# Performance work log

Hardware: AMD Instinct MI355X
Metric: run time of the kernel (lower is better)

Reference implementation:

```python
import jax, jax.numpy as jnp
import numpy as np

N_NODES = 100000
N_EDGES = 1600000
D_FEAT = 256
UNITS = 128


def setup_inputs() -> dict:
    key = jax.random.key(0)
    k1, k2, k3, k4, k5 = jax.random.split(key, 5)
    x = jax.random.normal(k1, (N_NODES, D_FEAT), dtype=jnp.float32)
    # glorot-scale init for w (scale doesn't affect correctness checking)
    w = jax.random.normal(k2, (D_FEAT, UNITS), dtype=jnp.float32) * (2.0 / (D_FEAT + UNITS)) ** 0.5
    adj_src = jax.random.randint(k3, (N_EDGES,), 0, N_NODES, dtype=jnp.int64)
    adj_dst = jax.random.randint(k4, (N_EDGES,), 0, N_NODES, dtype=jnp.int64)
    adj_vals = jax.random.uniform(k5, (N_EDGES,), dtype=jnp.float32)
    return {"x": x, "w": w, "adj_src": adj_src, "adj_dst": adj_dst, "adj_vals": adj_vals}


def reference(x, w, adj_src, adj_dst, adj_vals):
    # x: [N, D], w: [D, U]  -> dense projection
    h = x @ w  # [N, U]
    # sparse_dense_matmul(adj_norm, h): out[i] = sum_j A[i,j] * h[j]
    # COO: edge e contributes adj_vals[e] * h[adj_src[e]] to row adj_dst[e]
    msgs = adj_vals[:, None] * h[adj_src]  # [E, U]
    out = jax.ops.segment_sum(msgs, adj_dst, num_segments=N_NODES)  # [N, U]
    return out
```

## Files before the change

### kernel.cpp

```cpp
#include <hip/hip_runtime.h>

#define D_FEAT 256
#define UNITS  128

#define NBITS  7
#define BINSZ  128
#define BINCAP 2432
#define MAXNB  800

typedef __attribute__((ext_vector_type(8))) short short8;
typedef __attribute__((ext_vector_type(4))) float floatx4;

__device__ inline ushort f2bf(float f) {
    uint u = __float_as_uint(f);
    uint r = u + 0x7FFF + ((u >> 16) & 1);
    return (ushort)(r >> 16);
}

__global__ __launch_bounds__(256) void wt_prep_kernel(const float* __restrict__ w,
                                                      ushort* __restrict__ wT) {
    int idx = blockIdx.x * 256 + threadIdx.x;
    int n = idx >> 8;
    int k = idx & 255;
    wT[n * 256 + k] = f2bf(w[(size_t)k * UNITS + n]);
}

__global__ __launch_bounds__(256, 2) void gemm_mfma2_kernel(const float* __restrict__ x,
                                                            const ushort* __restrict__ wT,
                                                            ushort* __restrict__ hb, int M) {
    const int tid  = threadIdx.x;
    const int wave = tid >> 6;
    const int lane = tid & 63;
    const int quad = lane >> 4;
    const int m16  = lane & 15;

    const int row  = blockIdx.x * 64 + wave * 16 + m16;
    const int rowc = row < M ? row : M - 1;
    const float* xr = x + (size_t)rowc * D_FEAT;

    float4 xv[16];
    #pragma unroll
    for (int s = 0; s < 8; ++s) {
        const float4* p = (const float4*)(xr + s * 32 + quad * 8);
        xv[2 * s]     = p[0];
        xv[2 * s + 1] = p[1];
    }

    short8 afrag[8];
    #pragma unroll
    for (int s = 0; s < 8; ++s) {
        float4 lo = xv[2 * s];
        float4 hi = xv[2 * s + 1];
        union { short8 v; ushort u[8]; } af;
        af.u[0] = f2bf(lo.x); af.u[1] = f2bf(lo.y);
        af.u[2] = f2bf(lo.z); af.u[3] = f2bf(lo.w);
        af.u[4] = f2bf(hi.x); af.u[5] = f2bf(hi.y);
        af.u[6] = f2bf(hi.z); af.u[7] = f2bf(hi.w);
        afrag[s] = af.v;
    }

    floatx4 acc[8] = {};
    #pragma unroll
    for (int s = 0; s < 8; ++s) {
        #pragma unroll
        for (int c = 0; c < 8; ++c) {
            short8 bfrag = *(const short8*)&wT[(c * 16 + m16) * 256 + s * 32 + quad * 8];
            acc[c] = __builtin_amdgcn_mfma_f32_16x16x32_bf16(afrag[s], bfrag, acc[c], 0, 0, 0);
        }
    }

    #pragma unroll
    for (int c = 0; c < 8; ++c) {
        #pragma unroll
        for (int i = 0; i < 4; ++i) {
            int r = blockIdx.x * 64 + wave * 16 + quad * 4 + i;
            if (r < M) hb[(size_t)r * UNITS + c * 16 + m16] = f2bf(acc[c][i]);
        }
    }
}

__global__ __launch_bounds__(1024) void coarse_scatter_kernel(const int* __restrict__ src,
                                                              const int* __restrict__ dst,
                                                              const float* __restrict__ vals,
                                                              int* __restrict__ cursor,
                                                              int2* __restrict__ staged,
                                                              int E, int NB, int chunk) {
    __shared__ int s_hist[MAXNB];
    __shared__ int s_base[MAXNB];

    const int tid = threadIdx.x;
    const int T   = 1024;
    const int e0 = blockIdx.x * chunk;
    const int e1 = min(E, e0 + chunk);

    for (int i = tid; i < NB; i += T) s_hist[i] = 0;
    __syncthreads();

    for (int e = e0 + tid; e < e1; e += T)
        atomicAdd(&s_hist[dst[e] >> NBITS], 1);
    __syncthreads();

    for (int b = tid; b < NB; b += T) {
        int c = s_hist[b];
        s_base[b] = (c > 0) ? atomicAdd(&cursor[b * 4], c) : 0;
    }
    __syncthreads();
    for (int i = tid; i < NB; i += T) s_hist[i] = 0;
    __syncthreads();

    for (int e = e0 + tid; e < e1; e += T) {
        int d = dst[e];
        int b = d >> NBITS;
        int r = s_base[b] + atomicAdd(&s_hist[b], 1);
        if (r < BINCAP) {
            int meta = src[e] | ((d & (BINSZ - 1)) << 20);
            staged[(size_t)b * BINCAP + r] = make_int2(meta, __float_as_int(vals[e]));
        }
    }
}

__global__ __launch_bounds__(256) void gather_sort_kernel(const int* __restrict__ cursor,
                                                          const int2* __restrict__ staged,
                                                          const ushort* __restrict__ hb,
                                                          float* __restrict__ out, int N) {
    __shared__ int2 sbuf[BINCAP];
    __shared__ int cnt[BINSZ], ofs[BINSZ], cur[BINSZ];
    __shared__ int gofs[16];

    const int b   = blockIdx.x;
    const int tid = threadIdx.x;

    int n = cursor[b * 4];
    if (n > BINCAP) n = BINCAP;

    for (int i = tid; i < BINSZ; i += 256) cnt[i] = 0;
    __syncthreads();

    const int2* sg = staged + (size_t)b * BINCAP;

    for (int i = tid; i < n; i += 256)
        atomicAdd(&cnt[(sg[i].x >> 20) & (BINSZ - 1)], 1);
    __syncthreads();

    if (tid < 16) {
        int s = 0;
        #pragma unroll
        for (int j = 0; j < 8; ++j) s += cnt[tid * 8 + j];
        gofs[tid] = s;
    }
    __syncthreads();
    if (tid == 0) {
        int run = 0;
        #pragma unroll
        for (int g = 0; g < 16; ++g) { int c = gofs[g]; gofs[g] = run; run += c; }
    }
    __syncthreads();
    if (tid < 16) {
        int run = gofs[tid];
        #pragma unroll
        for (int j = 0; j < 8; ++j) {
            int d = tid * 8 + j;
            int c = cnt[d];
            ofs[d] = run; cur[d] = run; run += c;
        }
    }
    __syncthreads();

    for (int i = tid; i < n; i += 256) {
        int2 e = sg[i];
        int pos = atomicAdd(&cur[(e.x >> 20) & (BINSZ - 1)], 1);
        sbuf[pos] = e;
    }
    __syncthreads();

    const int half = tid >> 5;
    const int lane = tid & 31;

    for (int d0 = 0; d0 < BINSZ; d0 += 8) {
        int d  = d0 + half;
        int dg = b * BINSZ + d;
        if (dg >= N) continue;
        int start = ofs[d];
        int c     = cnt[d];

        float a0 = 0.f, a1 = 0.f, a2 = 0.f, a3 = 0.f;
        float b0 = 0.f, b1 = 0.f, b2 = 0.f, b3 = 0.f;
        int j = 0;
        for (; j + 2 <= c; j += 2) {
            int2 ea = sbuf[start + j];
            int2 eb = sbuf[start + j + 1];
            uint2 ha = *(const uint2*)(hb + (size_t)(ea.x & 0xFFFFF) * UNITS + lane * 4);
            uint2 hc = *(const uint2*)(hb + (size_t)(eb.x & 0xFFFFF) * UNITS + lane * 4);
            float va = __int_as_float(ea.y);
            float vb = __int_as_float(eb.y);
            a0 += va * __uint_as_float(ha.x << 16);
            a1 += va * __uint_as_float(ha.x & 0xFFFF0000u);
            a2 += va * __uint_as_float(ha.y << 16);
            a3 += va * __uint_as_float(ha.y & 0xFFFF0000u);
            b0 += vb * __uint_as_float(hc.x << 16);
            b1 += vb * __uint_as_float(hc.x & 0xFFFF0000u);
            b2 += vb * __uint_as_float(hc.y << 16);
            b3 += vb * __uint_as_float(hc.y & 0xFFFF0000u);
        }
        if (j < c) {
            int2 ea = sbuf[start + j];
            uint2 ha = *(const uint2*)(hb + (size_t)(ea.x & 0xFFFFF) * UNITS + lane * 4);
            float va = __int_as_float(ea.y);
            a0 += va * __uint_as_float(ha.x << 16);
            a1 += va * __uint_as_float(ha.x & 0xFFFF0000u);
            a2 += va * __uint_as_float(ha.y << 16);
            a3 += va * __uint_as_float(ha.y & 0xFFFF0000u);
        }
        float4 r = make_float4(a0 + b0, a1 + b1, a2 + b2, a3 + b3);
        *(float4*)(out + (size_t)dg * UNITS + lane * 4) = r;
    }
}

extern "C" void kernel_launch(void* const* d_in, const int* in_sizes, int n_in,
                              void* d_out, int out_size, void* d_ws, size_t ws_size,
                              hipStream_t stream) {
    const float* x        = (const float*)d_in[0];
    const float* w        = (const float*)d_in[1];
    const int*   adj_src  = (const int*)d_in[2];
    const int*   adj_dst  = (const int*)d_in[3];
    const float* adj_vals = (const float*)d_in[4];
    float*       out      = (float*)d_out;

    const int M = in_sizes[0] / D_FEAT;
    const int E = in_sizes[2];
    const int NB = (M + BINSZ - 1) >> NBITS;

    char*   ws  = (char*)d_ws;
    ushort* hb  = (ushort*)ws;
    size_t  off = (size_t)M * UNITS * sizeof(ushort);
    off = (off + 255) & ~(size_t)255;
    ushort* wT  = (ushort*)(ws + off);
    off += (size_t)128 * 256 * sizeof(ushort);
    int*    cursor = (int*)(ws + off);
    off += (size_t)NB * 4 * sizeof(int);
    off = (off + 15) & ~(size_t)15;
    int2*   staged = (int2*)(ws + off);

    hipMemsetAsync(cursor, 0, (size_t)NB * 4 * sizeof(int), stream);

    wt_prep_kernel<<<128, 256, 0, stream>>>(w, wT);

    gemm_mfma2_kernel<<<(M + 63) / 64, 256, 0, stream>>>(x, wT, hb, M);

    const int NSCAT = 256;
    const int chunk = (E + NSCAT - 1) / NSCAT;
    coarse_scatter_kernel<<<NSCAT, 1024, 0, stream>>>(adj_src, adj_dst, adj_vals,
                                                      cursor, staged, E, NB, chunk);

    gather_sort_kernel<<<NB, 256, 0, stream>>>(cursor, staged, hb, out, M);
}
```

Baseline: 315.9 us.

## Stage fragment-ordered weights in LDS and prefetch next x tile in persistent GEMM

The weight matrix is now pre-permuted into MFMA fragment order so each lane reads a contiguous 16-byte chunk. Each GEMM block copies the full 64 KB of bf16 weights into shared memory once. Blocks then loop persistently over about three row tiles, loading the next tile of x while the MFMAs for the current tile run. This removes repeated strided global reads of the weights and hides x load latency. In exchange it uses 64 KB of LDS per block, which may limit occupancy, and it launches fewer blocks.

```diff
diff --git a/kernel.cpp b/kernel.cpp
--- a/kernel.cpp
+++ b/kernel.cpp
@@ -17,64 +17,101 @@
     return (ushort)(r >> 16);
 }
 
-__global__ __launch_bounds__(256) void wt_prep_kernel(const float* __restrict__ w,
-                                                      ushort* __restrict__ wT) {
+__global__ __launch_bounds__(256) void wf_prep_kernel(const float* __restrict__ w,
+                                                      ushort* __restrict__ wF) {
     int idx = blockIdx.x * 256 + threadIdx.x;
-    int n = idx >> 8;
-    int k = idx & 255;
-    wT[n * 256 + k] = f2bf(w[(size_t)k * UNITS + n]);
-}
-
-__global__ __launch_bounds__(256, 2) void gemm_mfma2_kernel(const float* __restrict__ x,
-                                                            const ushort* __restrict__ wT,
-                                                            ushort* __restrict__ hb, int M) {
+    int j    = idx & 7;
+    int i    = idx >> 3;
+    int lane = i & 63;
+    int c    = (i >> 6) & 7;
+    int s    = i >> 9;
+    int m16  = lane & 15;
+    int quad = lane >> 4;
+    int k = s * 32 + quad * 8 + j;
+    int n = c * 16 + m16;
+    wF[idx] = f2bf(w[(size_t)k * UNITS + n]);
+}
+
+__global__ __launch_bounds__(256, 2) void gemm_mfma3_kernel(const float* __restrict__ x,
+                                                            const ushort* __restrict__ wF,
+                                                            ushort* __restrict__ hb,
+                                                            int M, int T) {
+    __shared__ ushort wS[32768];
+
     const int tid  = threadIdx.x;
     const int wave = tid >> 6;
     const int lane = tid & 63;
     const int quad = lane >> 4;
     const int m16  = lane & 15;
 
-    const int row  = blockIdx.x * 64 + wave * 16 + m16;
-    const int rowc = row < M ? row : M - 1;
-    const float* xr = x + (size_t)rowc * D_FEAT;
-
+    {
+        const uint4* s4 = (const uint4*)wF;
+        uint4*       d4 = (uint4*)wS;
+        #pragma unroll
+        for (int i = 0; i < 16; ++i) d4[tid + i * 256] = s4[tid + i * 256];
+    }
+    __syncthreads();
+
+    const int gstride = gridDim.x;
+    int t = blockIdx.x;
     float4 xv[16];
-    #pragma unroll
-    for (int s = 0; s < 8; ++s) {
-        const float4* p = (const float4*)(xr + s * 32 + quad * 8);
-        xv[2 * s]     = p[0];
-        xv[2 * s + 1] = p[1];
-    }
-
-    short8 afrag[8];
-    #pragma unroll
-    for (int s = 0; s < 8; ++s) {
-        float4 lo = xv[2 * s];
-        float4 hi = xv[2 * s + 1];
-        union { short8 v; ushort u[8]; } af;
-        af.u[0] = f2bf(lo.x); af.u[1] = f2bf(lo.y);
-        af.u[2] = f2bf(lo.z); af.u[3] = f2bf(lo.w);
-        af.u[4] = f2bf(hi.x); af.u[5] = f2bf(hi.y);
-        af.u[6] = f2bf(hi.z); af.u[7] = f2bf(hi.w);
-        afrag[s] = af.v;
-    }
-
-    floatx4 acc[8] = {};
-    #pragma unroll
-    for (int s = 0; s < 8; ++s) {
+
+    {
+        int row  = t * 64 + wave * 16 + m16;
+        int rowc = row < M ? row : M - 1;
+        const float* xr = x + (size_t)rowc * D_FEAT;
+        #pragma unroll
+        for (int s = 0; s < 8; ++s) {
+            const float4* p = (const float4*)(xr + s * 32 + quad * 8);
+            xv[2 * s]     = p[0];
+            xv[2 * s + 1] = p[1];
+        }
+    }
+
+    for (; t < T; t += gstride) {
+        short8 afrag[8];
+        #pragma unroll
+        for (int s = 0; s < 8; ++s) {
+            float4 lo = xv[2 * s];
+            float4 hi = xv[2 * s + 1];
+            union { short8 v; ushort u[8]; } af;
+            af.u[0] = f2bf(lo.x); af.u[1] = f2bf(lo.y);
+            af.u[2] = f2bf(lo.z); af.u[3] = f2bf(lo.w);
+            af.u[4] = f2bf(hi.x); af.u[5] = f2bf(hi.y);
+            af.u[6] = f2bf(hi.z); af.u[7] = f2bf(hi.w);
+            afrag[s] = af.v;
+        }
+
+        int tn = t + gstride;
+        if (tn < T) {
+            int row  = tn * 64 + wave * 16 + m16;
+            int rowc = row < M ? row : M - 1;
+            const float* xr = x + (size_t)rowc * D_FEAT;
+            #pragma unroll
+            for (int s = 0; s < 8; ++s) {
+                const float4* p = (const float4*)(xr + s * 32 + quad * 8);
+                xv[2 * s]     = p[0];
+                xv[2 * s + 1] = p[1];
+            }
+        }
+
+        floatx4 acc[8] = {};
+        #pragma unroll
+        for (int s = 0; s < 8; ++s) {
+            #pragma unroll
+            for (int c = 0; c < 8; ++c) {
+                short8 bfrag = *(const short8*)&wS[((s * 8 + c) << 9) + (lane << 3)];
+                acc[c] = __builtin_amdgcn_mfma_f32_16x16x32_bf16(afrag[s], bfrag, acc[c], 0, 0, 0);
+            }
+        }
+
         #pragma unroll
         for (int c = 0; c < 8; ++c) {
-            short8 bfrag = *(const short8*)&wT[(c * 16 + m16) * 256 + s * 32 + quad * 8];
-            acc[c] = __builtin_amdgcn_mfma_f32_16x16x32_bf16(afrag[s], bfrag, acc[c], 0, 0, 0);
-        }
-    }
-
-    #pragma unroll
-    for (int c = 0; c < 8; ++c) {
-        #pragma unroll
-        for (int i = 0; i < 4; ++i) {
-            int r = blockIdx.x * 64 + wave * 16 + quad * 4 + i;
-            if (r < M) hb[(size_t)r * UNITS + c * 16 + m16] = f2bf(acc[c][i]);
+            #pragma unroll
+            for (int i = 0; i < 4; ++i) {
+                int r = t * 64 + wave * 16 + quad * 4 + i;
+                if (r < M) hb[(size_t)r * UNITS + c * 16 + m16] = f2bf(acc[c][i]);
+            }
         }
     }
 }
@@ -234,7 +271,7 @@
     ushort* hb  = (ushort*)ws;
     size_t  off = (size_t)M * UNITS * sizeof(ushort);
     off = (off + 255) & ~(size_t)255;
-    ushort* wT  = (ushort*)(ws + off);
+    ushort* wF  = (ushort*)(ws + off);
     off += (size_t)128 * 256 * sizeof(ushort);
     int*    cursor = (int*)(ws + off);
     off += (size_t)NB * 4 * sizeof(int);
@@ -243,9 +280,11 @@
 
     hipMemsetAsync(cursor, 0, (size_t)NB * 4 * sizeof(int), stream);
 
-    wt_prep_kernel<<<128, 256, 0, stream>>>(w, wT);
-
-    gemm_mfma2_kernel<<<(M + 63) / 64, 256, 0, stream>>>(x, wT, hb, M);
+    wf_prep_kernel<<<128, 256, 0, stream>>>(w, wF);
+
+    const int T = (M + 63) / 64;
+    const int grid = (T + 2) / 3;
+    gemm_mfma3_kernel<<<grid, 256, 0, stream>>>(x, wF, hb, M, T);
 
     const int NSCAT = 256;
     const int chunk = (E + NSCAT - 1) / NSCAT;
```

After: 346.7 us. 9.7% more time.
